# Optimization experiments

Measured on AMD Instinct MI355X. Metric: run time of the kernel, lower is better.

Reference implementation:

```python
import jax, jax.numpy as jnp
import numpy as np

B, N, D, H = 4, 4096, 1024, 16
DH = D // H              # 64
M = int(DH * np.log(DH))  # 266 random features (performer-pytorch default)
EPS = 1e-4


def softmax_kernel(t, proj, is_query):
    # t: [B,H,N,DH], proj: [M,DH]  -> [B,H,N,M]  (FAVOR+ positive features)
    dn = t.shape[-1] ** -0.25
    ratio = proj.shape[0] ** -0.5
    td = jnp.einsum('bhnd,md->bhnm', t * dn, proj)
    diag = 0.5 * (dn ** 2) * jnp.sum(t * t, axis=-1, keepdims=True)  # [B,H,N,1]
    if is_query:
        mx = jnp.max(td, axis=-1, keepdims=True)
    else:
        mx = jnp.max(td, axis=(-1, -2), keepdims=True)
    return ratio * (jnp.exp(td - diag - mx) + EPS)


def setup_inputs() -> dict:
    key = jax.random.key(0)
    ks = jax.random.split(key, 12)
    s = 0.02
    inp = {
        'x':   jax.random.normal(ks[0], (B, N, D), jnp.float32),
        'Wq':  jax.random.normal(ks[1], (D, D), jnp.float32) * s,
        'bq':  jnp.zeros((D,), jnp.float32),
        'Wk':  jax.random.normal(ks[2], (D, D), jnp.float32) * s,
        'bk':  jnp.zeros((D,), jnp.float32),
        'Wv':  jax.random.normal(ks[3], (D, D), jnp.float32) * s,
        'bv':  jnp.zeros((D,), jnp.float32),
        'Wo':  jax.random.normal(ks[4], (D, D), jnp.float32) * s,
        'bo':  jnp.zeros((D,), jnp.float32),
        'Wfc': jax.random.normal(ks[5], (D, D), jnp.float32) * s,
        'bfc': jnp.zeros((D,), jnp.float32),
        'proj': jax.random.normal(ks[6], (M, DH), jnp.float32),  # random feature projection (frozen)
    }
    return inp


def reference(x, Wq, bq, Wk, bk, Wv, bv, Wo, bo, Wfc, bfc, proj):
    b, n, d = x.shape
    def heads(t):  # [B,N,D] -> [B,H,N,DH]
        return t.reshape(b, n, H, DH).transpose(0, 2, 1, 3)
    q = heads(x @ Wq.T + bq)
    k = heads(x @ Wk.T + bk)
    v = heads(x @ Wv.T + bv)

    qp = softmax_kernel(q, proj, is_query=True)    # [B,H,N,M]
    kp = softmax_kernel(k, proj, is_query=False)   # [B,H,N,M]

    # non-causal linear attention: O(N*M*DH)
    k_sum = jnp.sum(kp, axis=-2)                               # [B,H,M]
    d_inv = 1.0 / jnp.einsum('bhnm,bhm->bhn', qp, k_sum)       # [B,H,N]
    context = jnp.einsum('bhnm,bhnd->bhmd', kp, v)             # [B,H,M,DH]
    out = jnp.einsum('bhmd,bhnm,bhn->bhnd', context, qp, d_inv)

    out = out.transpose(0, 2, 1, 3).reshape(b, n, d)           # merge heads
    h = out @ Wo.T + bo                                        # performer internal to_out
    return jax.nn.relu(h @ Wfc.T + bfc)                        # wrapper fc_out + ReLU
```

## Files before the change

kernel.cpp:

```cpp
#include <hip/hip_runtime.h>
#include <math.h>

#define B_ 4
#define N_ 4096
#define D_ 1024
#define H_ 16
#define DH_ 64
#define M_ 266
#define MP_ 320

#define DN_ 0.35355339059327373f
#define RATIO_ 0.06131393394849658f
#define EPS_ 1e-4f
#define KP_ 72
#define NSPLIT_ 16
#define PARTSZ_ ((size_t)64 * M_ * 64)

typedef __attribute__((ext_vector_type(8))) short bfrag;
typedef __attribute__((ext_vector_type(4))) float f4;

__device__ __forceinline__ unsigned f2ord(float f) {
    unsigned u = __float_as_uint(f);
    return (u & 0x80000000u) ? ~u : (u | 0x80000000u);
}
__device__ __forceinline__ float ord2f(unsigned u) {
    unsigned b = (u & 0x80000000u) ? (u & 0x7fffffffu) : ~u;
    return __uint_as_float(b);
}

__global__ void zero_kernel(float* __restrict__ p, int n) {
    int i = blockIdx.x * 256 + threadIdx.x;
    if (i < n) p[i] = 0.f;
}

__device__ __forceinline__ void split2pack(float x, float y, unsigned* hp, unsigned* lp) {
    unsigned ux = __float_as_uint(x), uy = __float_as_uint(y);
    float hx = __uint_as_float(ux & 0xffff0000u);
    float hy = __uint_as_float(uy & 0xffff0000u);
    float lx = x - hx, ly = y - hy;
    *hp = (ux >> 16) | (uy & 0xffff0000u);
    *lp = (__float_as_uint(lx) >> 16) | (__float_as_uint(ly) & 0xffff0000u);
}
__device__ __forceinline__ unsigned short bf16rne(float x) {
    unsigned u = __float_as_uint(x);
    return (unsigned short)((u + 0x7fffu + ((u >> 16) & 1u)) >> 16);
}

__global__ __launch_bounds__(256) void gemm3_nt(const float* __restrict__ A,
        const float* __restrict__ Bw, const float* __restrict__ bias,
        float* __restrict__ C, int Kdim, int Ncols, int relu)
{
    __shared__ __align__(16) unsigned short Ah[128 * 32];
    __shared__ __align__(16) unsigned short Al[128 * 32];
    __shared__ __align__(16) unsigned short Bh[128 * 32];
    __shared__ __align__(16) unsigned short Bl[128 * 32];

    int tid = threadIdx.x;
    int bm = blockIdx.y * 128;
    int bn = blockIdx.x * 128;
    int lane = tid & 63;
    int wv = tid >> 6;
    int wm = wv >> 1, wn = wv & 1;
    int ml = lane & 15, kq = lane >> 4;

    f4 acc[4][4];
    #pragma unroll
    for (int i = 0; i < 4; ++i)
        #pragma unroll
        for (int j = 0; j < 4; ++j)
            acc[i][j] = (f4){0.f, 0.f, 0.f, 0.f};

    for (int kt = 0; kt < Kdim; kt += 32) {
        __syncthreads();
        #pragma unroll
        for (int j = 0; j < 4; ++j) {
            int c = tid + 256 * j;
            int m = c >> 3, k4 = c & 7;
            int li = m * 32 + k4 * 4;
            unsigned h0, l0, h1, l1;
            const float4 a = *(const float4*)(A + (size_t)(bm + m) * Kdim + kt + k4 * 4);
            split2pack(a.x, a.y, &h0, &l0);
            split2pack(a.z, a.w, &h1, &l1);
            *(uint2*)&Ah[li] = make_uint2(h0, h1);
            *(uint2*)&Al[li] = make_uint2(l0, l1);
            const float4 b = *(const float4*)(Bw + (size_t)(bn + m) * Kdim + kt + k4 * 4);
            split2pack(b.x, b.y, &h0, &l0);
            split2pack(b.z, b.w, &h1, &l1);
            *(uint2*)&Bh[li] = make_uint2(h0, h1);
            *(uint2*)&Bl[li] = make_uint2(l0, l1);
        }
        __syncthreads();
        bfrag ah[4], al[4], bh[4], bl[4];
        #pragma unroll
        for (int i = 0; i < 4; ++i) {
            int arow = wm * 64 + i * 16 + ml;
            ah[i] = *(const bfrag*)&Ah[arow * 32 + kq * 8];
            al[i] = *(const bfrag*)&Al[arow * 32 + kq * 8];
            int brow = wn * 64 + i * 16 + ml;
            bh[i] = *(const bfrag*)&Bh[brow * 32 + kq * 8];
            bl[i] = *(const bfrag*)&Bl[brow * 32 + kq * 8];
        }
        #pragma unroll
        for (int mi = 0; mi < 4; ++mi)
            #pragma unroll
            for (int ni = 0; ni < 4; ++ni) {
                acc[mi][ni] = __builtin_amdgcn_mfma_f32_16x16x32_bf16(ah[mi], bh[ni], acc[mi][ni], 0, 0, 0);
                acc[mi][ni] = __builtin_amdgcn_mfma_f32_16x16x32_bf16(al[mi], bh[ni], acc[mi][ni], 0, 0, 0);
                acc[mi][ni] = __builtin_amdgcn_mfma_f32_16x16x32_bf16(ah[mi], bl[ni], acc[mi][ni], 0, 0, 0);
            }
    }
    #pragma unroll
    for (int ni = 0; ni < 4; ++ni) {
        int col = bn + wn * 64 + ni * 16 + ml;
        float bv = bias[col];
        #pragma unroll
        for (int mi = 0; mi < 4; ++mi) {
            int row0 = bm + wm * 64 + mi * 16 + kq * 4;
            #pragma unroll
            for (int r = 0; r < 4; ++r) {
                float o = acc[mi][ni][r] + bv;
                if (relu) o = fmaxf(o, 0.f);
                C[(size_t)(row0 + r) * Ncols + col] = o;
            }
        }
    }
}

__global__ __launch_bounds__(256) void gemm3_qkv(const float* __restrict__ A,
        const float* __restrict__ W0, const float* __restrict__ W1, const float* __restrict__ W2,
        const float* __restrict__ b0, const float* __restrict__ b1, const float* __restrict__ b2,
        float* __restrict__ C0, float* __restrict__ C1, float* __restrict__ C2)
{
    __shared__ __align__(16) unsigned short Ah[128 * 32];
    __shared__ __align__(16) unsigned short Al[128 * 32];
    __shared__ __align__(16) unsigned short Bh[128 * 32];
    __shared__ __align__(16) unsigned short Bl[128 * 32];

    int tid = threadIdx.x;
    int sel = blockIdx.x >> 3;
    int bn = (blockIdx.x & 7) * 128;
    int bm = blockIdx.y * 128;
    const float* Bw = (sel == 0) ? W0 : (sel == 1) ? W1 : W2;
    const float* bias = (sel == 0) ? b0 : (sel == 1) ? b1 : b2;
    float* C = (sel == 0) ? C0 : (sel == 1) ? C1 : C2;

    int lane = tid & 63;
    int wv = tid >> 6;
    int wm = wv >> 1, wn = wv & 1;
    int ml = lane & 15, kq = lane >> 4;

    f4 acc[4][4];
    #pragma unroll
    for (int i = 0; i < 4; ++i)
        #pragma unroll
        for (int j = 0; j < 4; ++j)
            acc[i][j] = (f4){0.f, 0.f, 0.f, 0.f};

    for (int kt = 0; kt < D_; kt += 32) {
        __syncthreads();
        #pragma unroll
        for (int j = 0; j < 4; ++j) {
            int c = tid + 256 * j;
            int m = c >> 3, k4 = c & 7;
            int li = m * 32 + k4 * 4;
            unsigned h0, l0, h1, l1;
            const float4 a = *(const float4*)(A + (size_t)(bm + m) * D_ + kt + k4 * 4);
            split2pack(a.x, a.y, &h0, &l0);
            split2pack(a.z, a.w, &h1, &l1);
            *(uint2*)&Ah[li] = make_uint2(h0, h1);
            *(uint2*)&Al[li] = make_uint2(l0, l1);
            const float4 b = *(const float4*)(Bw + (size_t)(bn + m) * D_ + kt + k4 * 4);
            split2pack(b.x, b.y, &h0, &l0);
            split2pack(b.z, b.w, &h1, &l1);
            *(uint2*)&Bh[li] = make_uint2(h0, h1);
            *(uint2*)&Bl[li] = make_uint2(l0, l1);
        }
        __syncthreads();
        bfrag ah[4], al[4], bh[4], bl[4];
        #pragma unroll
        for (int i = 0; i < 4; ++i) {
            int arow = wm * 64 + i * 16 + ml;
            ah[i] = *(const bfrag*)&Ah[arow * 32 + kq * 8];
            al[i] = *(const bfrag*)&Al[arow * 32 + kq * 8];
            int brow = wn * 64 + i * 16 + ml;
            bh[i] = *(const bfrag*)&Bh[brow * 32 + kq * 8];
            bl[i] = *(const bfrag*)&Bl[brow * 32 + kq * 8];
        }
        #pragma unroll
        for (int mi = 0; mi < 4; ++mi)
            #pragma unroll
            for (int ni = 0; ni < 4; ++ni) {
                acc[mi][ni] = __builtin_amdgcn_mfma_f32_16x16x32_bf16(ah[mi], bh[ni], acc[mi][ni], 0, 0, 0);
                acc[mi][ni] = __builtin_amdgcn_mfma_f32_16x16x32_bf16(al[mi], bh[ni], acc[mi][ni], 0, 0, 0);
                acc[mi][ni] = __builtin_amdgcn_mfma_f32_16x16x32_bf16(ah[mi], bl[ni], acc[mi][ni], 0, 0, 0);
            }
    }
    #pragma unroll
    for (int ni = 0; ni < 4; ++ni) {
        int col = bn + wn * 64 + ni * 16 + ml;
        float bv = bias[col];
        #pragma unroll
        for (int mi = 0; mi < 4; ++mi) {
            int row0 = bm + wm * 64 + mi * 16 + kq * 4;
            #pragma unroll
            for (int r = 0; r < 4; ++r)
                C[(size_t)(row0 + r) * D_ + col] = acc[mi][ni][r] + bv;
        }
    }
}

__global__ __launch_bounds__(256) void kside(
    const float* __restrict__ Kin, const float* __restrict__ Vin,
    const float* __restrict__ proj,
    float* __restrict__ S_u, float* __restrict__ Cpart, float* __restrict__ C_u,
    float* __restrict__ Vsum, unsigned int* __restrict__ mxp)
{
    __shared__ __align__(16) unsigned short Kh[64 * KP_];
    __shared__ __align__(16) unsigned short VT[64 * KP_];
    __shared__ __align__(16) unsigned short Ph[2][64 * KP_];
    __shared__ __align__(16) unsigned short Us[64 * KP_];
    __shared__ __align__(16) float Ssum[MP_];
    __shared__ float diag[64];
    float* redf = (float*)Us;

    int bh = blockIdx.y, b = bh >> 4, h = bh & 15;
    int s = blockIdx.x;
    int n0 = s * 256;
    int tid = threadIdx.x, lane = tid & 63, w = tid >> 6;
    int ml = lane & 15, quad = lane >> 4;

    float* dstC = (s < NSPLIT_ - 1) ? (Cpart + (size_t)s * PARTSZ_) : C_u;

    for (int i = tid; i < MP_; i += 256) Ssum[i] = 0.f;

    f4 acc[5][4];
    #pragma unroll
    for (int i = 0; i < 5; ++i)
        #pragma unroll
        for (int j = 0; j < 4; ++j) acc[i][j] = (f4){0.f, 0.f, 0.f, 0.f};
    float vs[4] = {0.f, 0.f, 0.f, 0.f};
    float lmax = -1e30f;

    for (int nc = 0; nc < 4; ++nc) {
        __syncthreads();
        #pragma unroll
        for (int l = 0; l < 4; ++l) {
            int idx = tid + 256 * l;
            int r = idx >> 4;
            int d4 = (idx & 15) * 4;
            size_t g = ((size_t)(b * N_ + n0 + nc * 64 + r)) * D_ + h * DH_ + d4;
            const float4 kv = *(const float4*)(Kin + g);
            redf[r * 17 + (tid & 15)] = kv.x * kv.x + kv.y * kv.y + kv.z * kv.z + kv.w * kv.w;
            unsigned w0 = (unsigned)bf16rne(kv.x * DN_) | ((unsigned)bf16rne(kv.y * DN_) << 16);
            unsigned w1 = (unsigned)bf16rne(kv.z * DN_) | ((unsigned)bf16rne(kv.w * DN_) << 16);
            *(uint2*)&Kh[r * KP_ + d4] = make_uint2(w0, w1);
            const float4 vv = *(const float4*)(Vin + g);
            vs[0] += vv.x; vs[1] += vv.y; vs[2] += vv.z; vs[3] += vv.w;
            VT[(d4 + 0) * KP_ + r] = bf16rne(vv.x);
            VT[(d4 + 1) * KP_ + r] = bf16rne(vv.y);
            VT[(d4 + 2) * KP_ + r] = bf16rne(vv.z);
            VT[(d4 + 3) * KP_ + r] = bf16rne(vv.w);
        }
        {
            #pragma unroll
            for (int l = 0; l < 2; ++l) {
                int idx = tid + 256 * l;
                int m = idx >> 3, d8 = (idx & 7) * 8;
                const float4 p0 = *(const float4*)(proj + m * 64 + d8);
                const float4 p1 = *(const float4*)(proj + m * 64 + d8 + 4);
                unsigned a0 = (unsigned)bf16rne(p0.x) | ((unsigned)bf16rne(p0.y) << 16);
                unsigned a1 = (unsigned)bf16rne(p0.z) | ((unsigned)bf16rne(p0.w) << 16);
                unsigned a2 = (unsigned)bf16rne(p1.x) | ((unsigned)bf16rne(p1.y) << 16);
                unsigned a3 = (unsigned)bf16rne(p1.z) | ((unsigned)bf16rne(p1.w) << 16);
                *(uint4*)&Ph[0][m * KP_ + d8] = make_uint4(a0, a1, a2, a3);
            }
        }
        __syncthreads();
        if (tid < 64) {
            float ss = 0.f;
            #pragma unroll
            for (int p = 0; p < 16; ++p) ss += redf[tid * 17 + p];
            diag[tid] = ss * 0.0625f;
        }
        __syncthreads();

        bfrag kh0 = *(const bfrag*)&Kh[(w * 16 + ml) * KP_ + quad * 8];
        bfrag kh1 = *(const bfrag*)&Kh[(w * 16 + ml) * KP_ + 32 + quad * 8];
        float dgv[4];
        #pragma unroll
        for (int r = 0; r < 4; ++r) dgv[r] = diag[w * 16 + quad * 4 + r];

        for (int mc = 0; mc < 5; ++mc) {
            int pb = mc & 1;
            float4 pf[4];
            if (mc < 4) {
                #pragma unroll
                for (int l = 0; l < 2; ++l) {
                    int idx = tid + 256 * l;
                    int m = idx >> 3, d8 = (idx & 7) * 8;
                    int mg = (mc + 1) * 64 + m;
                    if (mg < M_) {
                        pf[l * 2 + 0] = *(const float4*)(proj + mg * 64 + d8);
                        pf[l * 2 + 1] = *(const float4*)(proj + mg * 64 + d8 + 4);
                    } else {
                        pf[l * 2 + 0] = make_float4(0.f, 0.f, 0.f, 0.f);
                        pf[l * 2 + 1] = make_float4(0.f, 0.f, 0.f, 0.f);
                    }
                }
            }
            #pragma unroll
            for (int mt = 0; mt < 4; ++mt) {
                int mrow = mt * 16 + ml;
                bfrag ph0 = *(const bfrag*)&Ph[pb][mrow * KP_ + quad * 8];
                bfrag ph1 = *(const bfrag*)&Ph[pb][mrow * KP_ + 32 + quad * 8];
                f4 t = (f4){0.f, 0.f, 0.f, 0.f};
                t = __builtin_amdgcn_mfma_f32_16x16x32_bf16(kh0, ph0, t, 0, 0, 0);
                t = __builtin_amdgcn_mfma_f32_16x16x32_bf16(kh1, ph1, t, 0, 0, 0);
                bool mv = (mc * 64 + mrow) < M_;
                float su = 0.f;
                unsigned short up[4];
                #pragma unroll
                for (int r = 0; r < 4; ++r) {
                    float u = 0.f;
                    if (mv) {
                        float tt = t[r];
                        lmax = fmaxf(lmax, tt);
                        u = __expf(tt - dgv[r]);
                    }
                    su += u;
                    up[r] = bf16rne(u);
                }
                su += __shfl_xor(su, 16);
                su += __shfl_xor(su, 32);
                if (mv && quad == 0) atomicAdd(&Ssum[mc * 64 + mrow], su);
                unsigned w0 = (unsigned)up[0] | ((unsigned)up[1] << 16);
                unsigned w1 = (unsigned)up[2] | ((unsigned)up[3] << 16);
                *(uint2*)&Us[mrow * KP_ + w * 16 + quad * 4] = make_uint2(w0, w1);
            }
            if (mc < 4) {
                #pragma unroll
                for (int l = 0; l < 2; ++l) {
                    int idx = tid + 256 * l;
                    int m = idx >> 3, d8 = (idx & 7) * 8;
                    const float4 p0 = pf[l * 2 + 0], p1 = pf[l * 2 + 1];
                    unsigned a0 = (unsigned)bf16rne(p0.x) | ((unsigned)bf16rne(p0.y) << 16);
                    unsigned a1 = (unsigned)bf16rne(p0.z) | ((unsigned)bf16rne(p0.w) << 16);
                    unsigned a2 = (unsigned)bf16rne(p1.x) | ((unsigned)bf16rne(p1.y) << 16);
                    unsigned a3 = (unsigned)bf16rne(p1.z) | ((unsigned)bf16rne(p1.w) << 16);
                    *(uint4*)&Ph[1 - pb][m * KP_ + d8] = make_uint4(a0, a1, a2, a3);
                }
            }
            __syncthreads();
            bfrag ua0 = *(const bfrag*)&Us[(w * 16 + ml) * KP_ + quad * 8];
            bfrag ua1 = *(const bfrag*)&Us[(w * 16 + ml) * KP_ + 32 + quad * 8];
            #pragma unroll
            for (int dt = 0; dt < 4; ++dt) {
                bfrag vb0 = *(const bfrag*)&VT[(dt * 16 + ml) * KP_ + quad * 8];
                bfrag vb1 = *(const bfrag*)&VT[(dt * 16 + ml) * KP_ + 32 + quad * 8];
                acc[mc][dt] = __builtin_amdgcn_mfma_f32_16x16x32_bf16(ua0, vb0, acc[mc][dt], 0, 0, 0);
                acc[mc][dt] = __builtin_amdgcn_mfma_f32_16x16x32_bf16(ua1, vb1, acc[mc][dt], 0, 0, 0);
            }
            __syncthreads();
        }
    }
    #pragma unroll
    for (int mc = 0; mc < 5; ++mc)
        #pragma unroll
        for (int dt = 0; dt < 4; ++dt)
            #pragma unroll
            for (int r = 0; r < 4; ++r) {
                int m = mc * 64 + w * 16 + quad * 4 + r;
                if (m < M_)
                    dstC[((size_t)bh * M_ + m) * 64 + dt * 16 + ml] = acc[mc][dt][r];
            }
    __syncthreads();
    for (int m = tid; m < M_; m += 256)
        atomicAdd(S_u + bh * M_ + m, Ssum[m]);
    #pragma unroll
    for (int off = 32; off; off >>= 1) lmax = fmaxf(lmax, __shfl_xor(lmax, off));
    __syncthreads();
    if (lane == 0) redf[w] = lmax;
    __syncthreads();
    if (tid == 0) {
        float mxv = fmaxf(fmaxf(redf[0], redf[1]), fmaxf(redf[2], redf[3]));
        atomicMax(mxp + bh, f2ord(mxv));
    }
    for (int j = 0; j < 4; ++j) {
        __syncthreads();
        redf[tid] = vs[j];
        __syncthreads();
        if (tid < 16) {
            float ss = 0.f;
            #pragma unroll
            for (int p = 0; p < 16; ++p) ss += redf[tid + 16 * p];
            atomicAdd(Vsum + bh * 64 + tid * 4 + j, ss);
        }
    }
}

__global__ __launch_bounds__(256) void finalize_kernel(
    const float* __restrict__ S_u, const float* __restrict__ Cpart, const float* __restrict__ C_u,
    const float* __restrict__ Vsum, const unsigned* __restrict__ mxp,
    float* __restrict__ ksum_f, unsigned short* __restrict__ ctxTh,
    unsigned short* __restrict__ ctxTl, float* __restrict__ Cs, float* __restrict__ kss)
{
    __shared__ float T[64 * 65];
    __shared__ float red[256];
    int mc = blockIdx.x, bh = blockIdx.y;
    int tid = threadIdx.x;
    float emx = __expf(-ord2f(mxp[bh]));

    float csacc = 0.f;
    #pragma unroll
    for (int i = 0; i < 16; ++i) {
        int idx = i * 256 + tid;
        int dh = idx & 63, mloc = idx >> 6;
        int m = mc * 64 + mloc;
        float v = 0.f;
        if (m < M_) {
            size_t off = ((size_t)bh * M_ + m) * 64 + dh;
            float sacc = C_u[off];
            for (int sp = 0; sp < NSPLIT_ - 1; ++sp)
                sacc += Cpart[(size_t)sp * PARTSZ_ + off];
            v = RATIO_ * (emx * sacc + EPS_ * Vsum[bh * 64 + dh]);
        }
        T[mloc * 65 + dh] = v;
        csacc += v;
    }
    red[tid] = csacc;
    __syncthreads();
    if (tid < 64) atomicAdd(&Cs[bh * 64 + tid], red[tid] + red[tid + 64] + red[tid + 128] + red[tid + 192]);
    float ksl = 0.f;
    if (tid < 64) {
        int m = mc * 64 + tid;
        float kv = (m < M_) ? RATIO_ * (emx * S_u[bh * M_ + m] + EPS_ * (float)N_) : 0.f;
        ksum_f[bh * MP_ + m] = kv;
        ksl = kv;
    }
    __syncthreads();
    red[tid] = ksl;
    __syncthreads();
    if (tid == 0) {
        float ss = 0.f;
        for (int p = 0; p < 64; ++p) ss += red[p];
        atomicAdd(kss + bh, ss);
    }
    __syncthreads();
    #pragma unroll
    for (int i = 0; i < 8; ++i) {
        int idx = i * 256 + tid;
        int dh = idx >> 5, m2 = (idx & 31) * 2;
        float v0 = T[m2 * 65 + dh], v1 = T[(m2 + 1) * 65 + dh];
        unsigned u0 = __float_as_uint(v0), u1 = __float_as_uint(v1);
        float lo0 = v0 - __uint_as_float(u0 & 0xffff0000u);
        float lo1 = v1 - __uint_as_float(u1 & 0xffff0000u);
        size_t dst = ((size_t)(bh * 64 + dh)) * MP_ + mc * 64 + m2;
        *(unsigned*)&ctxTh[dst] = (u0 >> 16) | (u1 & 0xffff0000u);
        *(unsigned*)&ctxTl[dst] = (__float_as_uint(lo0) >> 16) | (__float_as_uint(lo1) & 0xffff0000u);
    }
}

__global__ __launch_bounds__(256) void qattn(
    const float* __restrict__ Q, const float* __restrict__ proj,
    const float* __restrict__ ksum_f, const unsigned short* __restrict__ ctxTh,
    const unsigned short* __restrict__ ctxTl,
    const float* __restrict__ Cs, const float* __restrict__ kss,
    float* __restrict__ attn)
{
    __shared__ __align__(16) unsigned short Qh[64 * KP_], Ql[64 * KP_];
    __shared__ __align__(16) unsigned short Ph[64 * KP_], Pl[64 * KP_];
    __shared__ __align__(16) unsigned short Uh[64 * KP_], Ul[64 * KP_];
    __shared__ __align__(16) float ks[MP_];
    __shared__ float diag[64];
    float* redf = (float*)Uh;

    int bh = blockIdx.y, b = bh >> 4, h = bh & 15;
    int n0 = blockIdx.x * 64;
    int tid = threadIdx.x, lane = tid & 63, w = tid >> 6;
    int ml = lane & 15, quad = lane >> 4;

    #pragma unroll
    for (int l = 0; l < 4; ++l) {
        int idx = tid + 256 * l;
        int r = idx >> 4, d4 = (idx & 15) * 4;
        size_t g = ((size_t)(b * N_ + n0 + r)) * D_ + h * DH_ + d4;
        const float4 qv = *(const float4*)(Q + g);
        redf[r * 17 + (tid & 15)] = qv.x * qv.x + qv.y * qv.y + qv.z * qv.z + qv.w * qv.w;
        unsigned h0, l0, h1, l1;
        split2pack(qv.x * DN_, qv.y * DN_, &h0, &l0);
        split2pack(qv.z * DN_, qv.w * DN_, &h1, &l1);
        *(uint2*)&Qh[r * KP_ + d4] = make_uint2(h0, h1);
        *(uint2*)&Ql[r * KP_ + d4] = make_uint2(l0, l1);
    }
    for (int m = tid; m < MP_; m += 256) ks[m] = ksum_f[bh * MP_ + m];
    __syncthreads();
    if (tid < 64) {
        float s = 0.f;
        #pragma unroll
        for (int p = 0; p < 16; ++p) s += redf[tid * 17 + p];
        diag[tid] = s * 0.0625f;
    }
    __syncthreads();

    bfrag qh0 = *(const bfrag*)&Qh[(w * 16 + ml) * KP_ + quad * 8];
    bfrag ql0 = *(const bfrag*)&Ql[(w * 16 + ml) * KP_ + quad * 8];
    bfrag qh1 = *(const bfrag*)&Qh[(w * 16 + ml) * KP_ + 32 + quad * 8];
    bfrag ql1 = *(const bfrag*)&Ql[(w * 16 + ml) * KP_ + 32 + quad * 8];
    float dg = diag[w * 16 + ml];
    float dacc = 0.f, tmax = -1e30f;
    f4 oacc[4];
    #pragma unroll
    for (int i = 0; i < 4; ++i) oacc[i] = (f4){0.f, 0.f, 0.f, 0.f};

    for (int mc = 0; mc < 5; ++mc) {
        #pragma unroll
        for (int l = 0; l < 4; ++l) {
            int idx = tid + 256 * l;
            int m = idx >> 4, d4 = (idx & 15) * 4;
            int mg = mc * 64 + m;
            float4 p = make_float4(0.f, 0.f, 0.f, 0.f);
            if (mg < M_) p = *(const float4*)(proj + mg * 64 + d4);
            unsigned h0, l0, h1, l1;
            split2pack(p.x, p.y, &h0, &l0);
            split2pack(p.z, p.w, &h1, &l1);
            *(uint2*)&Ph[m * KP_ + d4] = make_uint2(h0, h1);
            *(uint2*)&Pl[m * KP_ + d4] = make_uint2(l0, l1);
        }
        __syncthreads();
        #pragma unroll
        for (int mt = 0; mt < 4; ++mt) {
            int mrow = mt * 16 + ml;
            bfrag ph0 = *(const bfrag*)&Ph[mrow * KP_ + quad * 8];
            bfrag pl0 = *(const bfrag*)&Pl[mrow * KP_ + quad * 8];
            bfrag ph1 = *(const bfrag*)&Ph[mrow * KP_ + 32 + quad * 8];
            bfrag pl1 = *(const bfrag*)&Pl[mrow * KP_ + 32 + quad * 8];
            f4 t = (f4){0.f, 0.f, 0.f, 0.f};
            t = __builtin_amdgcn_mfma_f32_16x16x32_bf16(ph0, qh0, t, 0, 0, 0);
            t = __builtin_amdgcn_mfma_f32_16x16x32_bf16(pl0, qh0, t, 0, 0, 0);
            t = __builtin_amdgcn_mfma_f32_16x16x32_bf16(ph0, ql0, t, 0, 0, 0);
            t = __builtin_amdgcn_mfma_f32_16x16x32_bf16(ph1, qh1, t, 0, 0, 0);
            t = __builtin_amdgcn_mfma_f32_16x16x32_bf16(pl1, qh1, t, 0, 0, 0);
            t = __builtin_amdgcn_mfma_f32_16x16x32_bf16(ph1, ql1, t, 0, 0, 0);
            const float4 ksv = *(const float4*)&ks[mc * 64 + mt * 16 + quad * 4];
            float ksa[4] = {ksv.x, ksv.y, ksv.z, ksv.w};
            unsigned short uh4[4], ul4[4];
            #pragma unroll
            for (int r = 0; r < 4; ++r) {
                int mg = mc * 64 + mt * 16 + quad * 4 + r;
                float tt = t[r];
                float u = __expf(tt - dg);
                if (mg < M_) tmax = fmaxf(tmax, tt);
                dacc = fmaf(u, ksa[r], dacc);
                unsigned uu = __float_as_uint(u);
                float lo = u - __uint_as_float(uu & 0xffff0000u);
                uh4[r] = (unsigned short)(uu >> 16);
                ul4[r] = (unsigned short)(__float_as_uint(lo) >> 16);
            }
            unsigned a0 = (unsigned)uh4[0] | ((unsigned)uh4[1] << 16);
            unsigned a1 = (unsigned)uh4[2] | ((unsigned)uh4[3] << 16);
            unsigned b0 = (unsigned)ul4[0] | ((unsigned)ul4[1] << 16);
            unsigned b1 = (unsigned)ul4[2] | ((unsigned)ul4[3] << 16);
            *(uint2*)&Uh[(w * 16 + ml) * KP_ + mt * 16 + quad * 4] = make_uint2(a0, a1);
            *(uint2*)&Ul[(w * 16 + ml) * KP_ + mt * 16 + quad * 4] = make_uint2(b0, b1);
        }
        __syncthreads();
        #pragma unroll
        for (int l = 0; l < 2; ++l) {
            int idx = tid + 256 * l;
            int dh = idx >> 3, m8 = (idx & 7) * 8;
            size_t src = ((size_t)(bh * 64 + dh)) * MP_ + mc * 64 + m8;
            *(uint4*)&Ph[dh * KP_ + m8] = *(const uint4*)(ctxTh + src);
            *(uint4*)&Pl[dh * KP_ + m8] = *(const uint4*)(ctxTl + src);
        }
        __syncthreads();
        bfrag ua0h = *(const bfrag*)&Uh[(w * 16 + ml) * KP_ + quad * 8];
        bfrag ua0l = *(const bfrag*)&Ul[(w * 16 + ml) * KP_ + quad * 8];
        bfrag ua1h = *(const bfrag*)&Uh[(w * 16 + ml) * KP_ + 32 + quad * 8];
        bfrag ua1l = *(const bfrag*)&Ul[(w * 16 + ml) * KP_ + 32 + quad * 8];
        #pragma unroll
        for (int dt = 0; dt < 4; ++dt) {
            bfrag cb0h = *(const bfrag*)&Ph[(dt * 16 + ml) * KP_ + quad * 8];
            bfrag cb0l = *(const bfrag*)&Pl[(dt * 16 + ml) * KP_ + quad * 8];
            bfrag cb1h = *(const bfrag*)&Ph[(dt * 16 + ml) * KP_ + 32 + quad * 8];
            bfrag cb1l = *(const bfrag*)&Pl[(dt * 16 + ml) * KP_ + 32 + quad * 8];
            oacc[dt] = __builtin_amdgcn_mfma_f32_16x16x32_bf16(ua0h, cb0h, oacc[dt], 0, 0, 0);
            oacc[dt] = __builtin_amdgcn_mfma_f32_16x16x32_bf16(ua0l, cb0h, oacc[dt], 0, 0, 0);
            oacc[dt] = __builtin_amdgcn_mfma_f32_16x16x32_bf16(ua0h, cb0l, oacc[dt], 0, 0, 0);
            oacc[dt] = __builtin_amdgcn_mfma_f32_16x16x32_bf16(ua1h, cb1h, oacc[dt], 0, 0, 0);
            oacc[dt] = __builtin_amdgcn_mfma_f32_16x16x32_bf16(ua1l, cb1h, oacc[dt], 0, 0, 0);
            oacc[dt] = __builtin_amdgcn_mfma_f32_16x16x32_bf16(ua1h, cb1l, oacc[dt], 0, 0, 0);
        }
        __syncthreads();
    }
    dacc += __shfl_xor(dacc, 16); dacc += __shfl_xor(dacc, 32);
    tmax = fmaxf(tmax, __shfl_xor(tmax, 16));
    tmax = fmaxf(tmax, __shfl_xor(tmax, 32));
    float fac = EPS_ * __expf(tmax);
    float dinv = 1.f / (dacc + fac * kss[bh]);
    #pragma unroll
    for (int dt = 0; dt < 4; ++dt) {
        float csv = Cs[bh * 64 + dt * 16 + ml];
        #pragma unroll
        for (int r = 0; r < 4; ++r) {
            int srcl = quad * 4 + r;
            float dv = __shfl(dinv, srcl);
            float fv = __shfl(fac, srcl);
            float o = (oacc[dt][r] + fv * csv) * dv;
            int n = n0 + w * 16 + quad * 4 + r;
            attn[((size_t)(b * N_ + n)) * D_ + h * DH_ + dt * 16 + ml] = o;
        }
    }
}

extern "C" void kernel_launch(void* const* d_in, const int* in_sizes, int n_in,
                              void* d_out, int out_size, void* d_ws, size_t ws_size,
                              hipStream_t stream)
{
    const float* x    = (const float*)d_in[0];
    const float* Wq   = (const float*)d_in[1];
    const float* bq   = (const float*)d_in[2];
    const float* Wk   = (const float*)d_in[3];
    const float* bk   = (const float*)d_in[4];
    const float* Wv   = (const float*)d_in[5];
    const float* bv   = (const float*)d_in[6];
    const float* Wo   = (const float*)d_in[7];
    const float* bo   = (const float*)d_in[8];
    const float* Wfc  = (const float*)d_in[9];
    const float* bfc  = (const float*)d_in[10];
    const float* proj = (const float*)d_in[11];
    float* out = (float*)d_out;

    float* ws = (float*)d_ws;
    const size_t nTok = (size_t)B_ * N_ * D_;
    const size_t nSu  = 64 * M_;
    const size_t nCu  = (size_t)64 * M_ * 64;
    const size_t nVs  = 64 * 64;
    const size_t nMx  = 64;
    const size_t nKsf = 64 * MP_;
    const size_t nCtx = (size_t)64 * MP_ * 64;
    const size_t nCs  = 64 * 64;

    const size_t offQ   = 0;
    const size_t offK   = nTok;
    const size_t offV   = nTok * 2;
    const size_t offSu  = nTok * 3;
    const size_t offCu  = offSu + nSu;
    const size_t offVs  = offCu + nCu;
    const size_t offMx  = offVs + nVs;
    const size_t offKsf = offMx + nMx;
    const size_t offCtx = offKsf + nKsf;
    const size_t offCs  = offCtx + nCtx;
    const size_t offKss = offCs + nCs;

    float* Q    = ws + offQ;
    float* Kb   = ws + offK;
    float* Vb   = ws + offV;
    float* S_u  = ws + offSu;
    float* C_u  = ws + offCu;
    float* Vsum = ws + offVs;
    unsigned* mx = (unsigned*)(ws + offMx);
    float* ksf  = ws + offKsf;
    unsigned short* ctxTh = (unsigned short*)(ws + offCtx);
    unsigned short* ctxTl = ctxTh + (size_t)64 * 64 * MP_;
    float* Cs   = ws + offCs;
    float* kss  = ws + offKss;
    float* attn = Kb;
    float* hbuf = Vb;
    float* Cpart = out;

    int nzero = (int)(nSu + nCu + nVs + nMx + nKsf + nCtx + nCs + 64);
    zero_kernel<<<dim3((nzero + 255) / 256), dim3(256), 0, stream>>>(S_u, nzero);

    gemm3_qkv<<<dim3(24, (B_ * N_) / 128), dim3(256), 0, stream>>>(
        x, Wq, Wk, Wv, bq, bk, bv, Q, Kb, Vb);

    kside<<<dim3(NSPLIT_, 64), dim3(256), 0, stream>>>(Kb, Vb, proj, S_u, Cpart, C_u, Vsum, mx);
    finalize_kernel<<<dim3(5, 64), dim3(256), 0, stream>>>(S_u, Cpart, C_u, Vsum, mx, ksf, ctxTh, ctxTl, Cs, kss);
    qattn<<<dim3(64, 64), dim3(256), 0, stream>>>(Q, proj, ksf, ctxTh, ctxTl, Cs, kss, attn);

    dim3 gg(D_ / 128, (B_ * N_) / 128);
    gemm3_nt<<<gg, dim3(256), 0, stream>>>(attn, Wo, bo, hbuf, D_, D_, 0);
    gemm3_nt<<<gg, dim3(256), 0, stream>>>(hbuf, Wfc, bfc, out, D_, D_, 1);
}
```

Baseline: 1.044 ms.

## Pre-split GEMM operands into bf16 hi/lo and load tiles via async global-to-LDS

Activations and weights are split into bf16 high/low halves once, in dedicated kernels or in the producing kernel's epilogue (qattn and the Wo GEMM), rather than being re-split inside every GEMM tile load. The GEMMs then stream the pre-split bf16 data straight into LDS with global_load_lds, which removes per-tile ALU conversion and register staging. The cost is extra split kernels and extra global traffic writing the split copies of x and all five weight matrices each call, plus more workspace use.

```diff
diff --git a/kernel.cpp b/kernel.cpp
--- a/kernel.cpp
+++ b/kernel.cpp
@@ -46,22 +46,68 @@
     return (unsigned short)((u + 0x7fffu + ((u >> 16) & 1u)) >> 16);
 }
 
-__global__ __launch_bounds__(256) void gemm3_nt(const float* __restrict__ A,
-        const float* __restrict__ Bw, const float* __restrict__ bias,
-        float* __restrict__ C, int Kdim, int Ncols, int relu)
+__device__ __forceinline__ void async_cp16(const void* g, void* l) {
+    __builtin_amdgcn_global_load_lds(
+        (const __attribute__((address_space(1))) void*)g,
+        (__attribute__((address_space(3))) void*)l, 16, 0, 0);
+}
+
+__global__ __launch_bounds__(256) void split_f32(const float* __restrict__ X,
+        unsigned short* __restrict__ Xh, unsigned short* __restrict__ Xl, int n4)
 {
-    __shared__ __align__(16) unsigned short Ah[128 * 32];
-    __shared__ __align__(16) unsigned short Al[128 * 32];
-    __shared__ __align__(16) unsigned short Bh[128 * 32];
-    __shared__ __align__(16) unsigned short Bl[128 * 32];
+    int i = blockIdx.x * 256 + threadIdx.x;
+    if (i >= n4) return;
+    const float4 v = ((const float4*)X)[i];
+    unsigned h0, l0, h1, l1;
+    split2pack(v.x, v.y, &h0, &l0);
+    split2pack(v.z, v.w, &h1, &l1);
+    ((uint2*)Xh)[i] = make_uint2(h0, h1);
+    ((uint2*)Xl)[i] = make_uint2(l0, l1);
+}
+
+__global__ __launch_bounds__(256) void split_w5(const float* __restrict__ W0,
+        const float* __restrict__ W1, const float* __restrict__ W2,
+        const float* __restrict__ W3, const float* __restrict__ W4,
+        unsigned short* __restrict__ Wsp)
+{
+    int sel = blockIdx.y;
+    const float* W = (sel == 0) ? W0 : (sel == 1) ? W1 : (sel == 2) ? W2 : (sel == 3) ? W3 : W4;
+    unsigned short* h = Wsp + (size_t)sel * 2097152;
+    unsigned short* l = h + 1048576;
+    int i = blockIdx.x * 256 + threadIdx.x;
+    const float4 v = ((const float4*)W)[i];
+    unsigned h0, l0, h1, l1;
+    split2pack(v.x, v.y, &h0, &l0);
+    split2pack(v.z, v.w, &h1, &l1);
+    ((uint2*)h)[i] = make_uint2(h0, h1);
+    ((uint2*)l)[i] = make_uint2(l0, l1);
+}
+
+__global__ __launch_bounds__(256) void gemm_qkv_s(
+        const unsigned short* __restrict__ Ah, const unsigned short* __restrict__ Al,
+        const unsigned short* __restrict__ Wsp,
+        const float* __restrict__ b0, const float* __restrict__ b1, const float* __restrict__ b2,
+        float* __restrict__ C0, float* __restrict__ C1, float* __restrict__ C2)
+{
+    __shared__ __align__(16) unsigned short Ahs[128 * 32];
+    __shared__ __align__(16) unsigned short Als[128 * 32];
+    __shared__ __align__(16) unsigned short Bhs[128 * 32];
+    __shared__ __align__(16) unsigned short Bls[128 * 32];
 
     int tid = threadIdx.x;
+    int sel = blockIdx.x >> 3;
+    int bn = (blockIdx.x & 7) * 128;
     int bm = blockIdx.y * 128;
-    int bn = blockIdx.x * 128;
+    const unsigned short* Bh = Wsp + (size_t)sel * 2097152;
+    const unsigned short* Bl = Bh + 1048576;
+    const float* bias = (sel == 0) ? b0 : (sel == 1) ? b1 : b2;
+    float* C = (sel == 0) ? C0 : (sel == 1) ? C1 : C2;
+
     int lane = tid & 63;
-    int wv = tid >> 6;
-    int wm = wv >> 1, wn = wv & 1;
+    int w = tid >> 6;
+    int wm = w >> 1, wn = w & 1;
     int ml = lane & 15, kq = lane >> 4;
+    int rsub = lane >> 2, ksub = (lane & 3) * 8;
 
     f4 acc[4][4];
     #pragma unroll
@@ -70,35 +116,28 @@
         for (int j = 0; j < 4; ++j)
             acc[i][j] = (f4){0.f, 0.f, 0.f, 0.f};
 
-    for (int kt = 0; kt < Kdim; kt += 32) {
-        __syncthreads();
-        #pragma unroll
-        for (int j = 0; j < 4; ++j) {
-            int c = tid + 256 * j;
-            int m = c >> 3, k4 = c & 7;
-            int li = m * 32 + k4 * 4;
-            unsigned h0, l0, h1, l1;
-            const float4 a = *(const float4*)(A + (size_t)(bm + m) * Kdim + kt + k4 * 4);
-            split2pack(a.x, a.y, &h0, &l0);
-            split2pack(a.z, a.w, &h1, &l1);
-            *(uint2*)&Ah[li] = make_uint2(h0, h1);
-            *(uint2*)&Al[li] = make_uint2(l0, l1);
-            const float4 b = *(const float4*)(Bw + (size_t)(bn + m) * Kdim + kt + k4 * 4);
-            split2pack(b.x, b.y, &h0, &l0);
-            split2pack(b.z, b.w, &h1, &l1);
-            *(uint2*)&Bh[li] = make_uint2(h0, h1);
-            *(uint2*)&Bl[li] = make_uint2(l0, l1);
+    for (int kt = 0; kt < D_; kt += 32) {
+        __syncthreads();
+        #pragma unroll
+        for (int j = 0; j < 2; ++j) {
+            int row = w * 32 + j * 16;
+            size_t ga = (size_t)(bm + row + rsub) * D_ + kt + ksub;
+            size_t gb = (size_t)(bn + row + rsub) * D_ + kt + ksub;
+            async_cp16(Ah + ga, &Ahs[row * 32]);
+            async_cp16(Al + ga, &Als[row * 32]);
+            async_cp16(Bh + gb, &Bhs[row * 32]);
+            async_cp16(Bl + gb, &Bls[row * 32]);
         }
         __syncthreads();
         bfrag ah[4], al[4], bh[4], bl[4];
         #pragma unroll
         for (int i = 0; i < 4; ++i) {
             int arow = wm * 64 + i * 16 + ml;
-            ah[i] = *(const bfrag*)&Ah[arow * 32 + kq * 8];
-            al[i] = *(const bfrag*)&Al[arow * 32 + kq * 8];
+            ah[i] = *(const bfrag*)&Ahs[arow * 32 + kq * 8];
+            al[i] = *(const bfrag*)&Als[arow * 32 + kq * 8];
             int brow = wn * 64 + i * 16 + ml;
-            bh[i] = *(const bfrag*)&Bh[brow * 32 + kq * 8];
-            bl[i] = *(const bfrag*)&Bl[brow * 32 + kq * 8];
+            bh[i] = *(const bfrag*)&Bhs[brow * 32 + kq * 8];
+            bl[i] = *(const bfrag*)&Bls[brow * 32 + kq * 8];
         }
         #pragma unroll
         for (int mi = 0; mi < 4; ++mi)
@@ -117,37 +156,31 @@
         for (int mi = 0; mi < 4; ++mi) {
             int row0 = bm + wm * 64 + mi * 16 + kq * 4;
             #pragma unroll
-            for (int r = 0; r < 4; ++r) {
-                float o = acc[mi][ni][r] + bv;
-                if (relu) o = fmaxf(o, 0.f);
-                C[(size_t)(row0 + r) * Ncols + col] = o;
-            }
-        }
-    }
-}
-
-__global__ __launch_bounds__(256) void gemm3_qkv(const float* __restrict__ A,
-        const float* __restrict__ W0, const float* __restrict__ W1, const float* __restrict__ W2,
-        const float* __restrict__ b0, const float* __restrict__ b1, const float* __restrict__ b2,
-        float* __restrict__ C0, float* __restrict__ C1, float* __restrict__ C2)
+            for (int r = 0; r < 4; ++r)
+                C[(size_t)(row0 + r) * D_ + col] = acc[mi][ni][r] + bv;
+        }
+    }
+}
+
+__global__ __launch_bounds__(256) void gemm_nt_s(
+        const unsigned short* __restrict__ Ah, const unsigned short* __restrict__ Al,
+        const unsigned short* __restrict__ Bh, const unsigned short* __restrict__ Bl,
+        const float* __restrict__ bias, float* __restrict__ C,
+        unsigned short* __restrict__ Ch, unsigned short* __restrict__ Cl, int mode)
 {
-    __shared__ __align__(16) unsigned short Ah[128 * 32];
-    __shared__ __align__(16) unsigned short Al[128 * 32];
-    __shared__ __align__(16) unsigned short Bh[128 * 32];
-    __shared__ __align__(16) unsigned short Bl[128 * 32];
+    __shared__ __align__(16) unsigned short Ahs[128 * 32];
+    __shared__ __align__(16) unsigned short Als[128 * 32];
+    __shared__ __align__(16) unsigned short Bhs[128 * 32];
+    __shared__ __align__(16) unsigned short Bls[128 * 32];
 
     int tid = threadIdx.x;
-    int sel = blockIdx.x >> 3;
-    int bn = (blockIdx.x & 7) * 128;
+    int bn = blockIdx.x * 128;
     int bm = blockIdx.y * 128;
-    const float* Bw = (sel == 0) ? W0 : (sel == 1) ? W1 : W2;
-    const float* bias = (sel == 0) ? b0 : (sel == 1) ? b1 : b2;
-    float* C = (sel == 0) ? C0 : (sel == 1) ? C1 : C2;
-
     int lane = tid & 63;
-    int wv = tid >> 6;
-    int wm = wv >> 1, wn = wv & 1;
+    int w = tid >> 6;
+    int wm = w >> 1, wn = w & 1;
     int ml = lane & 15, kq = lane >> 4;
+    int rsub = lane >> 2, ksub = (lane & 3) * 8;
 
     f4 acc[4][4];
     #pragma unroll
@@ -159,32 +192,25 @@
     for (int kt = 0; kt < D_; kt += 32) {
         __syncthreads();
         #pragma unroll
-        for (int j = 0; j < 4; ++j) {
-            int c = tid + 256 * j;
-            int m = c >> 3, k4 = c & 7;
-            int li = m * 32 + k4 * 4;
-            unsigned h0, l0, h1, l1;
-            const float4 a = *(const float4*)(A + (size_t)(bm + m) * D_ + kt + k4 * 4);
-            split2pack(a.x, a.y, &h0, &l0);
-            split2pack(a.z, a.w, &h1, &l1);
-            *(uint2*)&Ah[li] = make_uint2(h0, h1);
-            *(uint2*)&Al[li] = make_uint2(l0, l1);
-            const float4 b = *(const float4*)(Bw + (size_t)(bn + m) * D_ + kt + k4 * 4);
-            split2pack(b.x, b.y, &h0, &l0);
-            split2pack(b.z, b.w, &h1, &l1);
-            *(uint2*)&Bh[li] = make_uint2(h0, h1);
-            *(uint2*)&Bl[li] = make_uint2(l0, l1);
+        for (int j = 0; j < 2; ++j) {
+            int row = w * 32 + j * 16;
+            size_t ga = (size_t)(bm + row + rsub) * D_ + kt + ksub;
+            size_t gb = (size_t)(bn + row + rsub) * D_ + kt + ksub;
+            async_cp16(Ah + ga, &Ahs[row * 32]);
+            async_cp16(Al + ga, &Als[row * 32]);
+            async_cp16(Bh + gb, &Bhs[row * 32]);
+            async_cp16(Bl + gb, &Bls[row * 32]);
         }
         __syncthreads();
         bfrag ah[4], al[4], bh[4], bl[4];
         #pragma unroll
         for (int i = 0; i < 4; ++i) {
             int arow = wm * 64 + i * 16 + ml;
-            ah[i] = *(const bfrag*)&Ah[arow * 32 + kq * 8];
-            al[i] = *(const bfrag*)&Al[arow * 32 + kq * 8];
+            ah[i] = *(const bfrag*)&Ahs[arow * 32 + kq * 8];
+            al[i] = *(const bfrag*)&Als[arow * 32 + kq * 8];
             int brow = wn * 64 + i * 16 + ml;
-            bh[i] = *(const bfrag*)&Bh[brow * 32 + kq * 8];
-            bl[i] = *(const bfrag*)&Bl[brow * 32 + kq * 8];
+            bh[i] = *(const bfrag*)&Bhs[brow * 32 + kq * 8];
+            bl[i] = *(const bfrag*)&Bls[brow * 32 + kq * 8];
         }
         #pragma unroll
         for (int mi = 0; mi < 4; ++mi)
@@ -203,8 +229,19 @@
         for (int mi = 0; mi < 4; ++mi) {
             int row0 = bm + wm * 64 + mi * 16 + kq * 4;
             #pragma unroll
-            for (int r = 0; r < 4; ++r)
-                C[(size_t)(row0 + r) * D_ + col] = acc[mi][ni][r] + bv;
+            for (int r = 0; r < 4; ++r) {
+                float o = acc[mi][ni][r] + bv;
+                size_t idx = (size_t)(row0 + r) * D_ + col;
+                if (mode == 2) {
+                    unsigned u = __float_as_uint(o);
+                    float lo = o - __uint_as_float(u & 0xffff0000u);
+                    Ch[idx] = (unsigned short)(u >> 16);
+                    Cl[idx] = (unsigned short)(__float_as_uint(lo) >> 16);
+                } else {
+                    if (mode == 1) o = fmaxf(o, 0.f);
+                    C[idx] = o;
+                }
+            }
         }
     }
 }
@@ -465,7 +502,7 @@
     const float* __restrict__ ksum_f, const unsigned short* __restrict__ ctxTh,
     const unsigned short* __restrict__ ctxTl,
     const float* __restrict__ Cs, const float* __restrict__ kss,
-    float* __restrict__ attn)
+    unsigned short* __restrict__ attnH, unsigned short* __restrict__ attnL)
 {
     __shared__ __align__(16) unsigned short Qh[64 * KP_], Ql[64 * KP_];
     __shared__ __align__(16) unsigned short Ph[64 * KP_], Pl[64 * KP_];
@@ -607,7 +644,11 @@
             float fv = __shfl(fac, srcl);
             float o = (oacc[dt][r] + fv * csv) * dv;
             int n = n0 + w * 16 + quad * 4 + r;
-            attn[((size_t)(b * N_ + n)) * D_ + h * DH_ + dt * 16 + ml] = o;
+            size_t gi = ((size_t)(b * N_ + n)) * D_ + h * DH_ + dt * 16 + ml;
+            unsigned u = __float_as_uint(o);
+            float lo = o - __uint_as_float(u & 0xffff0000u);
+            attnH[gi] = (unsigned short)(u >> 16);
+            attnL[gi] = (unsigned short)(__float_as_uint(lo) >> 16);
         }
     }
 }
@@ -651,6 +692,7 @@
     const size_t offCtx = offKsf + nKsf;
     const size_t offCs  = offCtx + nCtx;
     const size_t offKss = offCs + nCs;
+    const size_t offWsp = offKss + 64;
 
     float* Q    = ws + offQ;
     float* Kb   = ws + offK;
@@ -664,21 +706,34 @@
     unsigned short* ctxTl = ctxTh + (size_t)64 * 64 * MP_;
     float* Cs   = ws + offCs;
     float* kss  = ws + offKss;
-    float* attn = Kb;
-    float* hbuf = Vb;
+    unsigned short* Wsp = (unsigned short*)(ws + offWsp);
+
+    unsigned short* xh = (unsigned short*)out;
+    unsigned short* xl = xh + nTok;
+    unsigned short* attnH = (unsigned short*)Kb;
+    unsigned short* attnL = attnH + nTok;
+    unsigned short* hbH = (unsigned short*)Vb;
+    unsigned short* hbL = hbH + nTok;
     float* Cpart = out;
 
     int nzero = (int)(nSu + nCu + nVs + nMx + nKsf + nCtx + nCs + 64);
     zero_kernel<<<dim3((nzero + 255) / 256), dim3(256), 0, stream>>>(S_u, nzero);
 
-    gemm3_qkv<<<dim3(24, (B_ * N_) / 128), dim3(256), 0, stream>>>(
-        x, Wq, Wk, Wv, bq, bk, bv, Q, Kb, Vb);
+    split_f32<<<dim3(16384), dim3(256), 0, stream>>>(x, xh, xl, (int)(nTok / 4));
+    split_w5<<<dim3(1024, 5), dim3(256), 0, stream>>>(Wq, Wk, Wv, Wo, Wfc, Wsp);
+
+    gemm_qkv_s<<<dim3(24, (B_ * N_) / 128), dim3(256), 0, stream>>>(
+        xh, xl, Wsp, bq, bk, bv, Q, Kb, Vb);
 
     kside<<<dim3(NSPLIT_, 64), dim3(256), 0, stream>>>(Kb, Vb, proj, S_u, Cpart, C_u, Vsum, mx);
     finalize_kernel<<<dim3(5, 64), dim3(256), 0, stream>>>(S_u, Cpart, C_u, Vsum, mx, ksf, ctxTh, ctxTl, Cs, kss);
-    qattn<<<dim3(64, 64), dim3(256), 0, stream>>>(Q, proj, ksf, ctxTh, ctxTl, Cs, kss, attn);
+    qattn<<<dim3(64, 64), dim3(256), 0, stream>>>(Q, proj, ksf, ctxTh, ctxTl, Cs, kss, attnH, attnL);
 
     dim3 gg(D_ / 128, (B_ * N_) / 128);
-    gemm3_nt<<<gg, dim3(256), 0, stream>>>(attn, Wo, bo, hbuf, D_, D_, 0);
-    gemm3_nt<<<gg, dim3(256), 0, stream>>>(hbuf, Wfc, bfc, out, D_, D_, 1);
-}
+    gemm_nt_s<<<gg, dim3(256), 0, stream>>>(attnH, attnL,
+        Wsp + (size_t)3 * 2097152, Wsp + (size_t)3 * 2097152 + 1048576,
+        bo, (float*)nullptr, hbH, hbL, 2);
+    gemm_nt_s<<<gg, dim3(256), 0, stream>>>(hbH, hbL,
+        Wsp + (size_t)4 * 2097152, Wsp + (size_t)4 * 2097152 + 1048576,
+        bfc, out, (unsigned short*)nullptr, (unsigned short*)nullptr, 1);
+}
```

Result: faster. 993.3 us (-4.9%).
